# Kernel tuning notes

Hardware: AMD Instinct MI355X
Metric: run time of the kernel (lower is better)

## Reference

```python
import jax, jax.numpy as jnp
import numpy as np

B, L, D, C_RES, O = 16384, 9, 32, 128, 2


def setup_inputs() -> dict:
    key = jax.random.key(0)
    ks = jax.random.split(key, 12)
    s = 1.0 / np.sqrt(D)
    sh = 1.0 / np.sqrt(C_RES)
    return {
        "seq_embd": jax.random.normal(ks[0], (B, L, D), jnp.float32),
        # relpos buffer: one-hot relative position encoding, matching
        # get_relative_position_encoding_matrix(9, 32): index (i - j + 16) in 32 bins
        "relpos": jax.nn.one_hot(
            jnp.arange(L)[:, None] - jnp.arange(L)[None, :] + D // 2, D, dtype=jnp.float32
        ),
        "Wi": jax.random.uniform(ks[1], (D, D), jnp.float32, -s, s),
        "bi": jax.random.uniform(ks[2], (D,), jnp.float32, -s, s),
        "Wj": jax.random.uniform(ks[3], (D, D), jnp.float32, -s, s),
        "bj": jax.random.uniform(ks[4], (D,), jnp.float32, -s, s),
        "Wr": jax.random.uniform(ks[5], (D, D), jnp.float32, -s, s),
        "br": jax.random.uniform(ks[6], (D,), jnp.float32, -s, s),
        "W1": jax.random.uniform(ks[7], (D, C_RES), jnp.float32, -s, s),
        "b1": jax.random.uniform(ks[8], (C_RES,), jnp.float32, -s, s),
        "W2": jax.random.uniform(ks[9], (C_RES, O), jnp.float32, -sh, sh),
        "b2": jax.random.uniform(ks[10], (O,), jnp.float32, -sh, sh),
    }


def reference(seq_embd, relpos, Wi, bi, Wj, bj, Wr, br, W1, b1, W2, b2):
    # r: [1, L, L, D]
    r = (jnp.einsum("ijd,de->ije", relpos, Wr) + br)[None]
    # x: [B, L, 1, D], y: [B, 1, L, D]
    x = (jnp.einsum("bld,de->ble", seq_embd, Wi) + bi)[:, :, None, :]
    y = (jnp.einsum("bld,de->ble", seq_embd, Wj) + bj)[:, None, :, :]
    z = x + y + r                                  # [B, L, L, D] outer sum
    h = jax.nn.relu(jnp.einsum("bijd,dc->bijc", z, W1) + b1)  # [B, L, L, C_RES]
    p = jnp.einsum("bijc,co->bijo", h, W2) + b2    # [B, L, L, O]
    return p.sum(axis=(1, 2))                      # [B, O]
```

## Files before the change

kernel.cpp:

```cpp
#include <hip/hip_runtime.h>
#include <hip/hip_bf16.h>

#define BB 16384
#define LL 9
#define DD 32
#define CR 128

typedef float v2 __attribute__((ext_vector_type(2)));


__global__ void precomp_kernel(const float* __restrict__ relpos,
                               const float* __restrict__ Wi, const float* __restrict__ bi,
                               const float* __restrict__ Wj, const float* __restrict__ bj,
                               const float* __restrict__ Wr, const float* __restrict__ br,
                               const float* __restrict__ W1, const float* __restrict__ b1,
                               float* __restrict__ ws)
{
    __shared__ float rv[DD];
    float* A1 = ws;
    float* A2 = ws + DD * CR;
    float* WK = ws + 2 * DD * CR;

    const int c = threadIdx.x;
    const int blk = blockIdx.x;

    if (blk < 32) {
        const int d = blk;
        float s = 0.f;
        #pragma unroll
        for (int e = 0; e < DD; ++e) s = fmaf(Wi[d * DD + e], W1[e * CR + c], s);
        A1[d * CR + c] = s;
    } else if (blk < 64) {
        const int d = blk - 32;
        float s = 0.f;
        #pragma unroll
        for (int e = 0; e < DD; ++e) s = fmaf(Wj[d * DD + e], W1[e * CR + c], s);
        A2[d * CR + c] = s;
    } else {
        const int k = blk - 64;
        const int dk = k - 8;
        const int i = dk > 0 ? dk : 0;
        const int j = i - dk;
        if (c < DD) {
            float s = bi[c] + bj[c] + br[c];
            #pragma unroll
            for (int d = 0; d < DD; ++d)
                s = fmaf(relpos[(i * LL + j) * DD + d], Wr[d * DD + c], s);
            rv[c] = s;
        }
        __syncthreads();
        float s = b1[c];
        #pragma unroll
        for (int e = 0; e < DD; ++e) s = fmaf(rv[e], W1[e * CR + c], s);
        WK[k * CR + c] = s;
    }
}

__global__ __launch_bounds__(256)
__attribute__((amdgpu_waves_per_eu(2, 2)))
void outersum_main(const float* __restrict__ seq,
                   const float* __restrict__ ws,
                   const float* __restrict__ W2,
                   const float* __restrict__ b2,
                   float* __restrict__ out)
{
    const float* gA1 = ws;
    const float* gA2 = ws + DD * CR;
    const float* gWK = ws + 2 * DD * CR;

    const int lane = threadIdx.x & 63;
    const int wave = blockIdx.x * (blockDim.x >> 6) + (threadIdx.x >> 6);
    const int nw = (gridDim.x * blockDim.x) >> 6;
    const int cp = lane * 2;

    v2 a1[DD], a2[DD];
    #pragma unroll
    for (int d = 0; d < DD; ++d) {
        a1[d] = *(const v2*)(gA1 + d * CR + cp);
        a2[d] = *(const v2*)(gA2 + d * CR + cp);
    }
    v2 wk[17];
    #pragma unroll
    for (int k = 0; k < 17; ++k) wk[k] = *(const v2*)(gWK + k * CR + cp);

    const float4 w4 = *(const float4*)(W2 + 2 * cp);
    v2 w2o0; w2o0.x = w4.x; w2o0.y = w4.z;
    v2 w2o1; w2o1.x = w4.y; w2o1.y = w4.w;
    const float bias0 = 81.f * b2[0];
    const float bias1 = 81.f * b2[1];

    for (int b = wave; b < BB; b += nw) {
        const int bu = __builtin_amdgcn_readfirstlane(b);
        const float* __restrict__ sp = seq + (size_t)bu * (LL * DD);

        v2 U[LL], V[LL];
        #pragma unroll
        for (int i = 0; i < LL; ++i) {
            v2 u; u.x = 0.f; u.y = 0.f;
            v2 v; v.x = 0.f; v.y = 0.f;
            #pragma unroll
            for (int d = 0; d < DD; ++d) {
                const float s = sp[i * DD + d];
                v2 s2; s2.x = s; s2.y = s;
                u += s2 * a1[d];
                v += s2 * a2[d];
            }
            U[i] = u; V[i] = v;
        }

        v2 acc0; acc0.x = 0.f; acc0.y = 0.f;
        v2 acc1; acc1.x = 0.f; acc1.y = 0.f;
        #pragma unroll
        for (int i = 0; i < LL; ++i) {
            #pragma unroll
            for (int j = 0; j < LL; ++j) {
                v2 t = U[i] + V[j] + wk[i - j + 8];
                t.x = fmaxf(t.x, 0.f);
                t.y = fmaxf(t.y, 0.f);
                acc0 += t * w2o0;
                acc1 += t * w2o1;
            }
        }

        float r0 = acc0.x + acc0.y;
        float r1 = acc1.x + acc1.y;
        #pragma unroll
        for (int off = 32; off; off >>= 1) {
            r0 += __shfl_xor(r0, off, 64);
            r1 += __shfl_xor(r1, off, 64);
        }
        if (lane == 0) {
            float2 o; o.x = r0 + bias0; o.y = r1 + bias1;
            *(float2*)(out + (size_t)bu * 2) = o;
        }
    }
}

extern "C" void kernel_launch(void* const* d_in, const int* in_sizes, int n_in,
                              void* d_out, int out_size, void* d_ws, size_t ws_size,
                              hipStream_t stream)
{
    const float* seq    = (const float*)d_in[0];
    const float* relpos = (const float*)d_in[1];
    const float* Wi     = (const float*)d_in[2];
    const float* bi     = (const float*)d_in[3];
    const float* Wj     = (const float*)d_in[4];
    const float* bj     = (const float*)d_in[5];
    const float* Wr     = (const float*)d_in[6];
    const float* br     = (const float*)d_in[7];
    const float* W1     = (const float*)d_in[8];
    const float* b1     = (const float*)d_in[9];
    const float* W2     = (const float*)d_in[10];
    const float* b2     = (const float*)d_in[11];
    float* out = (float*)d_out;
    float* ws  = (float*)d_ws;

    precomp_kernel<<<81, 128, 0, stream>>>(relpos, Wi, bi, Wj, bj, Wr, br, W1, b1, ws);

    outersum_main<<<512, 256, 0, stream>>>(seq, ws, W2, b2, out);
}
```

Measured before the change: 151.1 us.

## Stage folded A1/A2 weights in LDS instead of registers, raise occupancy

The precomputed Wi·W1 and Wj·W1 matrices are now stored interleaved and copied into shared memory per block, instead of being held as 128 registers per thread. Each thread reads them from LDS inside the d loop. Dropping the waves-per-eu cap and doubling the grid to 1024 blocks lets more waves stay resident, and each wave now handles exactly 4 batch rows in a fixed loop. The channel-to-lane mapping changes from lane*2 to {lane, lane+64}, with W2 reads adjusted to match. The trade-off is extra LDS reads and a per-block 32KB LDS fill in exchange for lower register pressure and more latency hiding.

After: 185.0 us. 22.4% more time.

```diff
diff --git a/kernel.cpp b/kernel.cpp
--- a/kernel.cpp
+++ b/kernel.cpp
@@ -17,25 +17,22 @@
                                float* __restrict__ ws)
 {
     __shared__ float rv[DD];
-    float* A1 = ws;
-    float* A2 = ws + DD * CR;
-    float* WK = ws + 2 * DD * CR;
-
     const int c = threadIdx.x;
     const int blk = blockIdx.x;
+    const int cl = c & 63, ch = c >> 6;
 
     if (blk < 32) {
         const int d = blk;
         float s = 0.f;
         #pragma unroll
         for (int e = 0; e < DD; ++e) s = fmaf(Wi[d * DD + e], W1[e * CR + c], s);
-        A1[d * CR + c] = s;
+        ws[d * 256 + cl * 4 + ch] = s;
     } else if (blk < 64) {
         const int d = blk - 32;
         float s = 0.f;
         #pragma unroll
         for (int e = 0; e < DD; ++e) s = fmaf(Wj[d * DD + e], W1[e * CR + c], s);
-        A2[d * CR + c] = s;
+        ws[d * 256 + cl * 4 + 2 + ch] = s;
     } else {
         const int k = blk - 64;
         const int dk = k - 8;
@@ -52,73 +49,82 @@
         float s = b1[c];
         #pragma unroll
         for (int e = 0; e < DD; ++e) s = fmaf(rv[e], W1[e * CR + c], s);
-        WK[k * CR + c] = s;
+        ws[8192 + k * 128 + cl * 2 + ch] = s;
     }
 }
 
 __global__ __launch_bounds__(256)
-__attribute__((amdgpu_waves_per_eu(2, 2)))
 void outersum_main(const float* __restrict__ seq,
                    const float* __restrict__ ws,
                    const float* __restrict__ W2,
                    const float* __restrict__ b2,
                    float* __restrict__ out)
 {
-    const float* gA1 = ws;
-    const float* gA2 = ws + DD * CR;
-    const float* gWK = ws + 2 * DD * CR;
+    __shared__ float lds_ab[8192];
 
-    const int lane = threadIdx.x & 63;
-    const int wave = blockIdx.x * (blockDim.x >> 6) + (threadIdx.x >> 6);
-    const int nw = (gridDim.x * blockDim.x) >> 6;
-    const int cp = lane * 2;
+    const int tid = threadIdx.x;
+    {
+        const float4* src = (const float4*)ws;
+        float4* dst = (float4*)lds_ab;
+        #pragma unroll
+        for (int t = 0; t < 8; ++t) dst[tid + t * 256] = src[tid + t * 256];
+    }
+    __syncthreads();
 
-    v2 a1[DD], a2[DD];
+    const int lane = tid & 63;
+    const int wave = __builtin_amdgcn_readfirstlane((blockIdx.x * 256 + tid) >> 6);
+
+    v2 wk[17];
+    const float* wkg = ws + 8192;
     #pragma unroll
-    for (int d = 0; d < DD; ++d) {
-        a1[d] = *(const v2*)(gA1 + d * CR + cp);
-        a2[d] = *(const v2*)(gA2 + d * CR + cp);
-    }
-    v2 wk[17];
-    #pragma unroll
-    for (int k = 0; k < 17; ++k) wk[k] = *(const v2*)(gWK + k * CR + cp);
+    for (int k = 0; k < 17; ++k) wk[k] = *(const v2*)(wkg + k * 128 + lane * 2);
 
-    const float4 w4 = *(const float4*)(W2 + 2 * cp);
-    v2 w2o0; w2o0.x = w4.x; w2o0.y = w4.z;
-    v2 w2o1; w2o1.x = w4.y; w2o1.y = w4.w;
+    const float2 w2a = ((const float2*)W2)[lane];
+    const float2 w2b = ((const float2*)W2)[lane + 64];
+    v2 w2o0; w2o0.x = w2a.x; w2o0.y = w2b.x;
+    v2 w2o1; w2o1.x = w2a.y; w2o1.y = w2b.y;
     const float bias0 = 81.f * b2[0];
     const float bias1 = 81.f * b2[1];
 
-    for (int b = wave; b < BB; b += nw) {
-        const int bu = __builtin_amdgcn_readfirstlane(b);
-        const float* __restrict__ sp = seq + (size_t)bu * (LL * DD);
+    #pragma unroll 1
+    for (int bi = 0; bi < 4; ++bi) {
+        const int b = wave + bi * 4096;
+        const float* __restrict__ sp = seq + (size_t)b * (LL * DD);
 
         v2 U[LL], V[LL];
         #pragma unroll
-        for (int i = 0; i < LL; ++i) {
-            v2 u; u.x = 0.f; u.y = 0.f;
-            v2 v; v.x = 0.f; v.y = 0.f;
+        for (int i = 0; i < LL; ++i) { U[i] = (v2)0.f; V[i] = (v2)0.f; }
+
+        #pragma unroll
+        for (int d = 0; d < DD; ++d) {
+            const float4 ab = *(const float4*)&lds_ab[(d * 64 + lane) * 4];
+            v2 a1p; a1p.x = ab.x; a1p.y = ab.y;
+            v2 a2p; a2p.x = ab.z; a2p.y = ab.w;
             #pragma unroll
-            for (int d = 0; d < DD; ++d) {
+            for (int i = 0; i < LL; ++i) {
                 const float s = sp[i * DD + d];
                 v2 s2; s2.x = s; s2.y = s;
-                u += s2 * a1[d];
-                v += s2 * a2[d];
+                U[i] += s2 * a1p;
+                V[i] += s2 * a2p;
             }
-            U[i] = u; V[i] = v;
         }
 
-        v2 acc0; acc0.x = 0.f; acc0.y = 0.f;
-        v2 acc1; acc1.x = 0.f; acc1.y = 0.f;
+        v2 acc0 = (v2)0.f, acc1 = (v2)0.f;
         #pragma unroll
-        for (int i = 0; i < LL; ++i) {
+        for (int k = 0; k < 17; ++k) {
+            const int dk = k - 8;
+            const int i0 = dk > 0 ? dk : 0;
+            const int cnt = LL - (dk > 0 ? dk : -dk);
+            const v2 w = wk[k];
             #pragma unroll
-            for (int j = 0; j < LL; ++j) {
-                v2 t = U[i] + V[j] + wk[i - j + 8];
-                t.x = fmaxf(t.x, 0.f);
-                t.y = fmaxf(t.y, 0.f);
-                acc0 += t * w2o0;
-                acc1 += t * w2o1;
+            for (int t = 0; t < cnt; ++t) {
+                const int i = i0 + t;
+                const int j = i - dk;
+                v2 tt = U[i] + V[j] + w;
+                tt.x = fmaxf(tt.x, 0.f);
+                tt.y = fmaxf(tt.y, 0.f);
+                acc0 += tt * w2o0;
+                acc1 += tt * w2o1;
             }
         }
 
@@ -131,7 +137,7 @@
         }
         if (lane == 0) {
             float2 o; o.x = r0 + bias0; o.y = r1 + bias1;
-            *(float2*)(out + (size_t)bu * 2) = o;
+            *(float2*)(out + (size_t)b * 2) = o;
         }
     }
 }
@@ -157,5 +163,5 @@
 
     precomp_kernel<<<81, 128, 0, stream>>>(relpos, Wi, bi, Wj, bj, Wr, br, W1, b1, ws);
 
-    outersum_main<<<512, 256, 0, stream>>>(seq, ws, W2, b2, out);
+    outersum_main<<<1024, 256, 0, stream>>>(seq, ws, W2, b2, out);
 }
```

## Load sequence rows as float4 per lane and double the grid

Applied to the files above, without the earlier changes.

Removes the two-waves-per-EU occupancy attribute and launches 1024 blocks so each wave handles a contiguous batch of 4 rows instead of grid-striding. The sequence row is now read as float4 vector loads through a VGPR offset, with an empty asm forcing the offset into a vector register, instead of scalar per-element loads. The intent is wider memory transactions and more occupancy to hide latency. The cost is redundant per-lane vector loads of the same data where scalar loads were used before, plus higher VGPR pressure.

Measured after the change: 139.2 us. 7.9% less time.

```diff
diff --git a/kernel.cpp b/kernel.cpp
--- a/kernel.cpp
+++ b/kernel.cpp
@@ -57,7 +57,6 @@
 }
 
 __global__ __launch_bounds__(256)
-__attribute__((amdgpu_waves_per_eu(2, 2)))
 void outersum_main(const float* __restrict__ seq,
                    const float* __restrict__ ws,
                    const float* __restrict__ W2,
@@ -69,8 +68,7 @@
     const float* gWK = ws + 2 * DD * CR;
 
     const int lane = threadIdx.x & 63;
-    const int wave = blockIdx.x * (blockDim.x >> 6) + (threadIdx.x >> 6);
-    const int nw = (gridDim.x * blockDim.x) >> 6;
+    const int wave_id = blockIdx.x * 4 + (threadIdx.x >> 6);
     const int cp = lane * 2;
 
     v2 a1[DD], a2[DD];
@@ -89,27 +87,33 @@
     const float bias0 = 81.f * b2[0];
     const float bias1 = 81.f * b2[1];
 
-    for (int b = wave; b < BB; b += nw) {
-        const int bu = __builtin_amdgcn_readfirstlane(b);
-        const float* __restrict__ sp = seq + (size_t)bu * (LL * DD);
+    #pragma unroll 1
+    for (int p = 0; p < 4; ++p) {
+        const int b = wave_id * 4 + p;
+        int off4 = b * 72;
+        asm volatile("" : "+v"(off4));
+        const float4* sp4 = (const float4*)seq + off4;
 
         v2 U[LL], V[LL];
         #pragma unroll
         for (int i = 0; i < LL; ++i) {
-            v2 u; u.x = 0.f; u.y = 0.f;
-            v2 v; v.x = 0.f; v.y = 0.f;
+            v2 u = (v2)0.f, v = (v2)0.f;
             #pragma unroll
-            for (int d = 0; d < DD; ++d) {
-                const float s = sp[i * DD + d];
-                v2 s2; s2.x = s; s2.y = s;
-                u += s2 * a1[d];
-                v += s2 * a2[d];
+            for (int dc = 0; dc < 8; ++dc) {
+                const float4 s = sp4[i * 8 + dc];
+                u += (v2)(s.x) * a1[dc * 4 + 0];
+                v += (v2)(s.x) * a2[dc * 4 + 0];
+                u += (v2)(s.y) * a1[dc * 4 + 1];
+                v += (v2)(s.y) * a2[dc * 4 + 1];
+                u += (v2)(s.z) * a1[dc * 4 + 2];
+                v += (v2)(s.z) * a2[dc * 4 + 2];
+                u += (v2)(s.w) * a1[dc * 4 + 3];
+                v += (v2)(s.w) * a2[dc * 4 + 3];
             }
             U[i] = u; V[i] = v;
         }
 
-        v2 acc0; acc0.x = 0.f; acc0.y = 0.f;
-        v2 acc1; acc1.x = 0.f; acc1.y = 0.f;
+        v2 acc0 = (v2)0.f, acc1 = (v2)0.f;
         #pragma unroll
         for (int i = 0; i < LL; ++i) {
             #pragma unroll
@@ -125,13 +129,13 @@
         float r0 = acc0.x + acc0.y;
         float r1 = acc1.x + acc1.y;
         #pragma unroll
-        for (int off = 32; off; off >>= 1) {
-            r0 += __shfl_xor(r0, off, 64);
-            r1 += __shfl_xor(r1, off, 64);
+        for (int offx = 32; offx; offx >>= 1) {
+            r0 += __shfl_xor(r0, offx, 64);
+            r1 += __shfl_xor(r1, offx, 64);
         }
         if (lane == 0) {
             float2 o; o.x = r0 + bias0; o.y = r1 + bias1;
-            *(float2*)(out + (size_t)bu * 2) = o;
+            *(float2*)(out + (size_t)b * 2) = o;
         }
     }
 }
@@ -157,5 +161,5 @@
 
     precomp_kernel<<<81, 128, 0, stream>>>(relpos, Wi, bi, Wj, bj, Wr, br, W1, b1, ws);
 
-    outersum_main<<<512, 256, 0, stream>>>(seq, ws, W2, b2, out);
+    outersum_main<<<1024, 256, 0, stream>>>(seq, ws, W2, b2, out);
 }
```

## Process four batches per wave, stream projection weights, defer W2 multiply

Applied to the files above, without the earlier changes.

Each wave now handles four consecutive batch rows. It loads the A1/A2 projection weights in chunks of four rather than keeping all 64 pairs resident in registers, and it computes U/V with inline v_pk_fma_f32 using op_sel to broadcast scalars. The pairwise loop sums only the ReLU outputs per channel, and the W2 projection is applied once at the end, so each (i,j,channel) costs one packed add instead of two packed FMAs. The grid is resized to cover exactly one set of four rows per wave. In exchange, register pressure rises from holding 4×9 U/V pairs, and the fixed grid mapping assumes B is divisible by 16384.

New measurement: 191.4 us. 1.27x slower.

```diff
diff --git a/kernel.cpp b/kernel.cpp
--- a/kernel.cpp
+++ b/kernel.cpp
@@ -7,6 +7,24 @@
 #define CR 128
 
 typedef float v2 __attribute__((ext_vector_type(2)));
+
+__device__ __forceinline__ v2 pk_fma_lo(v2 s, v2 a, v2 c) {
+    v2 d;
+    asm("v_pk_fma_f32 %0, %1, %2, %3 op_sel:[0,0,0] op_sel_hi:[0,1,1]"
+        : "=v"(d) : "v"(s), "v"(a), "v"(c));
+    return d;
+}
+__device__ __forceinline__ v2 pk_fma_hi(v2 s, v2 a, v2 c) {
+    v2 d;
+    asm("v_pk_fma_f32 %0, %1, %2, %3 op_sel:[1,0,0] op_sel_hi:[1,1,1]"
+        : "=v"(d) : "v"(s), "v"(a), "v"(c));
+    return d;
+}
+__device__ __forceinline__ v2 pk_add(v2 a, v2 b) {
+    v2 d;
+    asm("v_pk_add_f32 %0, %1, %2" : "=v"(d) : "v"(a), "v"(b));
+    return d;
+}
 
 
 __global__ void precomp_kernel(const float* __restrict__ relpos,
@@ -56,8 +74,7 @@
     }
 }
 
-__global__ __launch_bounds__(256)
-__attribute__((amdgpu_waves_per_eu(2, 2)))
+__global__ __launch_bounds__(256, 2)
 void outersum_main(const float* __restrict__ seq,
                    const float* __restrict__ ws,
                    const float* __restrict__ W2,
@@ -69,61 +86,77 @@
     const float* gWK = ws + 2 * DD * CR;
 
     const int lane = threadIdx.x & 63;
-    const int wave = blockIdx.x * (blockDim.x >> 6) + (threadIdx.x >> 6);
-    const int nw = (gridDim.x * blockDim.x) >> 6;
+    const int wid  = blockIdx.x * 4 + (threadIdx.x >> 6);
     const int cp = lane * 2;
 
-    v2 a1[DD], a2[DD];
-    #pragma unroll
-    for (int d = 0; d < DD; ++d) {
-        a1[d] = *(const v2*)(gA1 + d * CR + cp);
-        a2[d] = *(const v2*)(gA2 + d * CR + cp);
-    }
     v2 wk[17];
     #pragma unroll
     for (int k = 0; k < 17; ++k) wk[k] = *(const v2*)(gWK + k * CR + cp);
+    const float4 w4 = *(const float4*)(W2 + 2 * cp);
+    const float bias0 = 81.f * b2[0], bias1 = 81.f * b2[1];
 
-    const float4 w4 = *(const float4*)(W2 + 2 * cp);
-    v2 w2o0; w2o0.x = w4.x; w2o0.y = w4.z;
-    v2 w2o1; w2o1.x = w4.y; w2o1.y = w4.w;
-    const float bias0 = 81.f * b2[0];
-    const float bias1 = 81.f * b2[1];
+    int soff = wid * (4 * LL * DD);
+    asm volatile("" : "+v"(soff));
+    const float* sbase = seq + soff;
 
-    for (int b = wave; b < BB; b += nw) {
-        const int bu = __builtin_amdgcn_readfirstlane(b);
-        const float* __restrict__ sp = seq + (size_t)bu * (LL * DD);
+    v2 U[4][LL], V[4][LL];
+    #pragma unroll
+    for (int p = 0; p < 4; ++p)
+        #pragma unroll
+        for (int i = 0; i < LL; ++i) { U[p][i] = (v2)0.f; V[p][i] = (v2)0.f; }
 
-        v2 U[LL], V[LL];
+    #pragma unroll 1
+    for (int dc = 0; dc < 8; ++dc) {
+        v2 a1s[4], a2s[4];
         #pragma unroll
-        for (int i = 0; i < LL; ++i) {
-            v2 u; u.x = 0.f; u.y = 0.f;
-            v2 v; v.x = 0.f; v.y = 0.f;
+        for (int t = 0; t < 4; ++t) {
+            a1s[t] = *(const v2*)(gA1 + (dc * 4 + t) * CR + cp);
+            a2s[t] = *(const v2*)(gA2 + (dc * 4 + t) * CR + cp);
+        }
+        const float* sd = sbase + dc * 4;
+        #pragma unroll
+        for (int p = 0; p < 4; ++p) {
             #pragma unroll
-            for (int d = 0; d < DD; ++d) {
-                const float s = sp[i * DD + d];
-                v2 s2; s2.x = s; s2.y = s;
-                u += s2 * a1[d];
-                v += s2 * a2[d];
+            for (int i = 0; i < LL; ++i) {
+                const float4 s = *(const float4*)(sd + (p * LL + i) * DD);
+                v2 s01; s01.x = s.x; s01.y = s.y;
+                v2 s23; s23.x = s.z; s23.y = s.w;
+                U[p][i] = pk_fma_lo(s01, a1s[0], U[p][i]);
+                U[p][i] = pk_fma_hi(s01, a1s[1], U[p][i]);
+                U[p][i] = pk_fma_lo(s23, a1s[2], U[p][i]);
+                U[p][i] = pk_fma_hi(s23, a1s[3], U[p][i]);
+                V[p][i] = pk_fma_lo(s01, a2s[0], V[p][i]);
+                V[p][i] = pk_fma_hi(s01, a2s[1], V[p][i]);
+                V[p][i] = pk_fma_lo(s23, a2s[2], V[p][i]);
+                V[p][i] = pk_fma_hi(s23, a2s[3], V[p][i]);
             }
-            U[i] = u; V[i] = v;
         }
+    }
 
-        v2 acc0; acc0.x = 0.f; acc0.y = 0.f;
-        v2 acc1; acc1.x = 0.f; acc1.y = 0.f;
+    v2 q[4];
+    #pragma unroll
+    for (int p = 0; p < 4; ++p) q[p] = (v2)0.f;
+    #pragma unroll
+    for (int i = 0; i < LL; ++i) {
         #pragma unroll
-        for (int i = 0; i < LL; ++i) {
+        for (int j = 0; j < LL; ++j) {
+            const v2 w = wk[i - j + 8];
             #pragma unroll
-            for (int j = 0; j < LL; ++j) {
-                v2 t = U[i] + V[j] + wk[i - j + 8];
+            for (int p = 0; p < 4; ++p) {
+                v2 t = pk_add(U[p][i], V[p][j]);
+                t = pk_add(t, w);
                 t.x = fmaxf(t.x, 0.f);
                 t.y = fmaxf(t.y, 0.f);
-                acc0 += t * w2o0;
-                acc1 += t * w2o1;
+                q[p] = pk_add(q[p], t);
             }
         }
+    }
 
-        float r0 = acc0.x + acc0.y;
-        float r1 = acc1.x + acc1.y;
+    const int b0 = wid * 4;
+    #pragma unroll
+    for (int p = 0; p < 4; ++p) {
+        float r0 = fmaf(q[p].y, w4.z, q[p].x * w4.x);
+        float r1 = fmaf(q[p].y, w4.w, q[p].x * w4.y);
         #pragma unroll
         for (int off = 32; off; off >>= 1) {
             r0 += __shfl_xor(r0, off, 64);
@@ -131,7 +164,7 @@
         }
         if (lane == 0) {
             float2 o; o.x = r0 + bias0; o.y = r1 + bias1;
-            *(float2*)(out + (size_t)bu * 2) = o;
+            *(float2*)(out + (size_t)(b0 + p) * 2) = o;
         }
     }
 }
@@ -157,5 +190,5 @@
 
     precomp_kernel<<<81, 128, 0, stream>>>(relpos, Wi, bi, Wj, bj, Wr, br, W1, b1, ws);
 
-    outersum_main<<<512, 256, 0, stream>>>(seq, ws, W2, b2, out);
+    outersum_main<<<1024, 256, 0, stream>>>(seq, ws, W2, b2, out);
 }
```
